# Kernel tuning notes

Measured on AMD Instinct MI355X. Metric: run time of the kernel, lower is better.

The kernel has to match this reference:

```python
import jax, jax.numpy as jnp
import numpy as np

H = 64  # LSTM units for both layers
T = 128  # sequence length
D = 128  # input feature dim
B = 2048  # batch

def setup_inputs() -> dict:
    key = jax.random.key(0)
    ks = jax.random.split(key, 7)
    s_in = 1.0 / np.sqrt(D)
    s_h = 1.0 / np.sqrt(H)
    return {
        "x": jax.random.normal(ks[0], (B, T, D), dtype=jnp.float32),
        # Keras LSTM weights: kernel [in, 4H], recurrent_kernel [H, 4H], bias [4H]
        # gate order: i, f, g (cell candidate), o
        "W1": jax.random.normal(ks[1], (D, 4 * H), dtype=jnp.float32) * s_in,
        "U1": jax.random.normal(ks[2], (H, 4 * H), dtype=jnp.float32) * s_h,
        "b1": jnp.zeros((4 * H,), dtype=jnp.float32),
        "W2": jax.random.normal(ks[3], (H, 4 * H), dtype=jnp.float32) * s_h,
        "U2": jax.random.normal(ks[4], (H, 4 * H), dtype=jnp.float32) * s_h,
        "b2": jnp.zeros((4 * H,), dtype=jnp.float32),
    }

def _lstm(x, W, U, b, act):
    """Keras-faithful LSTM, return_sequences=True, zero init state.
    x: [B, T, D_in] -> hs: [B, T, H]
    recurrent_activation = sigmoid; `act` is the cell/output activation.
    """
    Bsz = x.shape[0]
    # Precompute input projections for all timesteps (one big GEMM).
    xz = jnp.einsum('btd,dg->btg', x, W) + b  # [B, T, 4H]
    xz = jnp.swapaxes(xz, 0, 1)  # [T, B, 4H]

    def step(carry, zt):
        h, c = carry
        z = zt + h @ U  # [B, 4H]
        i, f, g, o = jnp.split(z, 4, axis=-1)
        i = jax.nn.sigmoid(i)
        f = jax.nn.sigmoid(f)
        g = act(g)
        o = jax.nn.sigmoid(o)
        c = f * c + i * g
        h = o * act(c)
        return (h, c), h

    init = (jnp.zeros((Bsz, H), x.dtype), jnp.zeros((Bsz, H), x.dtype))
    _, hs = jax.lax.scan(step, init, xz)  # hs: [T, B, H]
    return jnp.swapaxes(hs, 0, 1)  # [B, T, H]

def reference(x, W1, U1, b1, W2, U2, b2):
    h1 = _lstm(x, W1, U1, b1, jnp.tanh)           # layer 1: default tanh
    h2 = _lstm(h1, W2, U2, b2, jax.nn.sigmoid)    # layer 2: activation='sigmoid'
    return h2.reshape(h2.shape[0], T * H, 1)      # Reshape((8192, 1))
```

## Files before the change

### kernel.cpp

```cpp
#include <hip/hip_runtime.h>
#include <stdint.h>

typedef __attribute__((ext_vector_type(8))) short short8;
typedef __attribute__((ext_vector_type(4))) short short4_t;
typedef __attribute__((ext_vector_type(4))) float floatx4;

#define TT 128
#define DD 128

#define BARRIER_LDS() asm volatile("s_waitcnt lgkmcnt(0)\n\ts_barrier" ::: "memory")

__device__ __forceinline__ short f2bf(float f) {
  union { float f; uint32_t u; } v; v.f = f;
  uint32_t u = v.u;
  u += 0x7fffu + ((u >> 16) & 1u);
  return (short)(u >> 16);
}

__device__ __forceinline__ float sigf(float x) {
  return __builtin_amdgcn_rcpf(1.f + __expf(-x));
}
__device__ __forceinline__ float tanhf_(float x) {
  return 2.f * __builtin_amdgcn_rcpf(1.f + __expf(-2.f * x)) - 1.f;
}

__global__ void wtrans_all(const float* __restrict__ W1, const float* __restrict__ U1,
                           const float* __restrict__ W2, const float* __restrict__ U2,
                           short* __restrict__ w1t, short* __restrict__ u1t,
                           short* __restrict__ w2t, short* __restrict__ u2t) {
  int n = blockIdx.x;
  int k = threadIdx.x;
  w1t[n * 128 + k] = f2bf(W1[k * 256 + n]);
  if (k < 64) {
    u1t[n * 64 + k] = f2bf(U1[k * 256 + n]);
    w2t[n * 64 + k] = f2bf(W2[k * 256 + n]);
    u2t[n * 64 + k] = f2bf(U2[k * 256 + n]);
  }
}

__global__ __launch_bounds__(512, 2) void lstm_fused(
    const float* __restrict__ x,
    const short* __restrict__ w1t, const short* __restrict__ u1t,
    const short* __restrict__ w2t, const short* __restrict__ u2t,
    const float* __restrict__ b1, const float* __restrict__ b2,
    float* __restrict__ out) {
  __shared__ short hb1[2][8 * 80];
  __shared__ short hb2[2][8 * 80];
  __shared__ short xbuf[2][8 * 144];

  const int tid = threadIdx.x;
  const int w = tid >> 6;
  const bool isL1 = (w < 4);
  const int wg = w & 3;
  const int lane = tid & 63;
  const int mrow = lane & 15;
  const int quad = lane >> 4;
  const int rowbase = blockIdx.x * 8;
  const int colw = wg * 16 + mrow;
  const int br_a = 2 * (mrow >> 2) + (mrow & 1);

  short8 wA[4][4], uA[4][2];
  float bias[4];
  if (isL1) {
#pragma unroll
    for (int g = 0; g < 4; ++g) {
      const int n = g * 4 + wg;
#pragma unroll
      for (int s = 0; s < 4; ++s)
        wA[g][s] = *(const short8*)(w1t + n * 2048 + mrow * 128 + quad * 8 + s * 32);
#pragma unroll
      for (int s = 0; s < 2; ++s)
        uA[g][s] = *(const short8*)(u1t + n * 1024 + mrow * 64 + quad * 8 + s * 32);
      bias[g] = b1[g * 64 + colw];
    }
  } else {
#pragma unroll
    for (int g = 0; g < 4; ++g) {
      const int n = g * 4 + wg;
#pragma unroll
      for (int s = 0; s < 2; ++s) {
        wA[g][s]     = *(const short8*)(w2t + n * 1024 + mrow * 64 + quad * 8 + s * 32);
        wA[g][2 + s] = *(const short8*)(u2t + n * 1024 + mrow * 64 + quad * 8 + s * 32);
      }
      bias[g] = b2[g * 64 + colw];
    }
  }

  const int tid2 = tid & 255;
  const int sxr = tid2 >> 5;
  const int sxc = (tid2 & 31) * 4;
  const float* xload = x + (size_t)(rowbase + sxr) * (TT * DD) + sxc;

  short8 h1f[2], xh[4];
  float cc[2] = {0.f, 0.f};
  floatx4 xcur, xnxt;

  for (int idx = tid; idx < 2 * 8 * 80; idx += 512) {
    ((short*)hb1)[idx] = 0;
    ((short*)hb2)[idx] = 0;
  }
  if (!isL1) {
    floatx4 x0 = *(const floatx4*)xload;
    short4_t v;
#pragma unroll
    for (int j = 0; j < 4; ++j) v[j] = f2bf(x0[j]);
    *(short4_t*)&xbuf[0][sxr * 144 + sxc] = v;
    xcur = *(const floatx4*)(xload + DD);
    xnxt = *(const floatx4*)(xload + 2 * DD);
  }
  BARRIER_LDS();

  float* outp = out + (size_t)rowbase * 8192 + colw;

#pragma unroll 1
  for (int i = 0; i <= TT; ++i) {
    const int p = i & 1;

    if (isL1) {
      if (i < TT) {
#pragma unroll
        for (int s = 0; s < 4; ++s)
          xh[s] = *(const short8*)&xbuf[p][br_a * 144 + (quad + 4 * s) * 8];
        h1f[0] = *(const short8*)&hb1[1 - p][br_a * 80 + quad * 8];
        h1f[1] = *(const short8*)&hb1[1 - p][br_a * 80 + (quad + 4) * 8];

        floatx4 acc[4];
#pragma unroll
        for (int g = 0; g < 4; ++g) acc[g] = floatx4{0.f, 0.f, 0.f, 0.f};
#pragma unroll
        for (int s = 0; s < 4; ++s)
#pragma unroll
          for (int g = 0; g < 4; ++g)
            acc[g] = __builtin_amdgcn_mfma_f32_16x16x32_bf16(xh[s], wA[g][s], acc[g], 0, 0, 0);
#pragma unroll
        for (int s = 0; s < 2; ++s)
#pragma unroll
          for (int g = 0; g < 4; ++g)
            acc[g] = __builtin_amdgcn_mfma_f32_16x16x32_bf16(h1f[s], uA[g][s], acc[g], 0, 0, 0);

#pragma unroll
        for (int r = 0; r < 2; ++r) {
          float ig = sigf(acc[0][r] + bias[0]);
          float fg = sigf(acc[1][r] + bias[1]);
          float gg = tanhf_(acc[2][r] + bias[2]);
          float og = sigf(acc[3][r] + bias[3]);
          float c = fg * cc[r] + ig * gg;
          cc[r] = c;
          float h = og * tanhf_(c);
          hb1[p][(2 * quad + r) * 80 + colw] = f2bf(h);
        }
      }
    } else {
      if (i >= 1) {
        h1f[0] = *(const short8*)&hb1[1 - p][br_a * 80 + quad * 8];
        h1f[1] = *(const short8*)&hb1[1 - p][br_a * 80 + (quad + 4) * 8];
        xh[0]  = *(const short8*)&hb2[1 - p][br_a * 80 + quad * 8];
        xh[1]  = *(const short8*)&hb2[1 - p][br_a * 80 + (quad + 4) * 8];

        floatx4 acc[4];
#pragma unroll
        for (int g = 0; g < 4; ++g) acc[g] = floatx4{0.f, 0.f, 0.f, 0.f};
#pragma unroll
        for (int s = 0; s < 2; ++s)
#pragma unroll
          for (int g = 0; g < 4; ++g)
            acc[g] = __builtin_amdgcn_mfma_f32_16x16x32_bf16(h1f[s], wA[g][s], acc[g], 0, 0, 0);
#pragma unroll
        for (int s = 0; s < 2; ++s)
#pragma unroll
          for (int g = 0; g < 4; ++g)
            acc[g] = __builtin_amdgcn_mfma_f32_16x16x32_bf16(xh[s], wA[g][2 + s], acc[g], 0, 0, 0);

        if (i <= TT - 2) {
          short4_t v;
#pragma unroll
          for (int j = 0; j < 4; ++j) v[j] = f2bf(xcur[j]);
          *(short4_t*)&xbuf[1 - p][sxr * 144 + sxc] = v;
          xcur = xnxt;
          const int tn = (i + 3 < TT) ? (i + 3) : (TT - 1);
          xnxt = *(const floatx4*)(xload + (size_t)tn * DD);
        }

        const int t = i - 1;
#pragma unroll
        for (int r = 0; r < 2; ++r) {
          float ig = sigf(acc[0][r] + bias[0]);
          float fg = sigf(acc[1][r] + bias[1]);
          float gg = sigf(acc[2][r] + bias[2]);
          float og = sigf(acc[3][r] + bias[3]);
          float c = fg * cc[r] + ig * gg;
          cc[r] = c;
          float h = og * sigf(c);
          hb2[p][(2 * quad + r) * 80 + colw] = f2bf(h);
          outp[(size_t)(2 * quad + r) * 8192 + t * 64] = h;
        }
      } else {
        short4_t v;
#pragma unroll
        for (int j = 0; j < 4; ++j) v[j] = f2bf(xcur[j]);
        *(short4_t*)&xbuf[1 - p][sxr * 144 + sxc] = v;
        xcur = xnxt;
        xnxt = *(const floatx4*)(xload + (size_t)3 * DD);
      }
    }

    BARRIER_LDS();
  }
}

extern "C" void kernel_launch(void* const* d_in, const int* in_sizes, int n_in,
                              void* d_out, int out_size, void* d_ws, size_t ws_size,
                              hipStream_t stream) {
  const float* x  = (const float*)d_in[0];
  const float* W1 = (const float*)d_in[1];
  const float* U1 = (const float*)d_in[2];
  const float* b1 = (const float*)d_in[3];
  const float* W2 = (const float*)d_in[4];
  const float* U2 = (const float*)d_in[5];
  const float* b2 = (const float*)d_in[6];
  float* out = (float*)d_out;

  short* w1t = (short*)d_ws;
  short* u1t = w1t + 32768;
  short* w2t = u1t + 16384;
  short* u2t = w2t + 16384;

  hipLaunchKernelGGL(wtrans_all, dim3(256), dim3(128), 0, stream,
                     W1, U1, W2, U2, w1t, u1t, w2t, u2t);
  hipLaunchKernelGGL(lstm_fused, dim3(256), dim3(512), 0, stream,
                     x, w1t, u1t, w2t, u2t, b1, b2, out);
}
```

Baseline: 327.7 us.

## Software-pipeline layer-1 input projection one step ahead of the recurrence

Layer-1 waves now compute the x·W input-projection MFMAs for step t+1 after finishing the gate update for step t, so each step's critical path holds only the recurrent h·U MFMAs. To support this, the layer-2 waves stage x into LDS one step further ahead, with a two-deep register prefetch and a prologue that preloads two timesteps. Scheduling fences are added before the barriers to keep the compiler from moving work across them. The accumulators now live across loop iterations, which raises register pressure under the 512-thread, 2-block launch bounds.

```diff
diff --git a/kernel.cpp b/kernel.cpp
--- a/kernel.cpp
+++ b/kernel.cpp
@@ -9,6 +9,7 @@
 #define DD 128
 
 #define BARRIER_LDS() asm volatile("s_waitcnt lgkmcnt(0)\n\ts_barrier" ::: "memory")
+#define SFENCE() __builtin_amdgcn_sched_barrier(0)
 
 __device__ __forceinline__ short f2bf(float f) {
   union { float f; uint32_t u; } v; v.f = f;
@@ -92,8 +93,9 @@
   const float* xload = x + (size_t)(rowbase + sxr) * (TT * DD) + sxc;
 
   short8 h1f[2], xh[4];
+  floatx4 acc[4];
   float cc[2] = {0.f, 0.f};
-  floatx4 xcur, xnxt;
+  floatx4 xn_a, xn_b;
 
   for (int idx = tid; idx < 2 * 8 * 80; idx += 512) {
     ((short*)hb1)[idx] = 0;
@@ -101,13 +103,31 @@
   }
   if (!isL1) {
     floatx4 x0 = *(const floatx4*)xload;
+    floatx4 x1 = *(const floatx4*)(xload + DD);
     short4_t v;
 #pragma unroll
     for (int j = 0; j < 4; ++j) v[j] = f2bf(x0[j]);
     *(short4_t*)&xbuf[0][sxr * 144 + sxc] = v;
-    xcur = *(const floatx4*)(xload + DD);
-    xnxt = *(const floatx4*)(xload + 2 * DD);
-  }
+#pragma unroll
+    for (int j = 0; j < 4; ++j) v[j] = f2bf(x1[j]);
+    *(short4_t*)&xbuf[1][sxr * 144 + sxc] = v;
+    xn_a = *(const floatx4*)(xload + 2 * DD);
+    xn_b = *(const floatx4*)(xload + 3 * DD);
+  }
+  BARRIER_LDS();
+  if (isL1) {
+#pragma unroll
+    for (int s = 0; s < 4; ++s)
+      xh[s] = *(const short8*)&xbuf[0][br_a * 144 + (quad + 4 * s) * 8];
+#pragma unroll
+    for (int g = 0; g < 4; ++g) acc[g] = floatx4{0.f, 0.f, 0.f, 0.f};
+#pragma unroll
+    for (int s = 0; s < 4; ++s)
+#pragma unroll
+      for (int g = 0; g < 4; ++g)
+        acc[g] = __builtin_amdgcn_mfma_f32_16x16x32_bf16(xh[s], wA[g][s], acc[g], 0, 0, 0);
+  }
+  SFENCE();
   BARRIER_LDS();
 
   float* outp = out + (size_t)rowbase * 8192 + colw;
@@ -118,26 +138,13 @@
 
     if (isL1) {
       if (i < TT) {
-#pragma unroll
-        for (int s = 0; s < 4; ++s)
-          xh[s] = *(const short8*)&xbuf[p][br_a * 144 + (quad + 4 * s) * 8];
         h1f[0] = *(const short8*)&hb1[1 - p][br_a * 80 + quad * 8];
         h1f[1] = *(const short8*)&hb1[1 - p][br_a * 80 + (quad + 4) * 8];
-
-        floatx4 acc[4];
-#pragma unroll
-        for (int g = 0; g < 4; ++g) acc[g] = floatx4{0.f, 0.f, 0.f, 0.f};
-#pragma unroll
-        for (int s = 0; s < 4; ++s)
-#pragma unroll
-          for (int g = 0; g < 4; ++g)
-            acc[g] = __builtin_amdgcn_mfma_f32_16x16x32_bf16(xh[s], wA[g][s], acc[g], 0, 0, 0);
 #pragma unroll
         for (int s = 0; s < 2; ++s)
 #pragma unroll
           for (int g = 0; g < 4; ++g)
             acc[g] = __builtin_amdgcn_mfma_f32_16x16x32_bf16(h1f[s], uA[g][s], acc[g], 0, 0, 0);
-
 #pragma unroll
         for (int r = 0; r < 2; ++r) {
           float ig = sigf(acc[0][r] + bias[0]);
@@ -150,14 +157,24 @@
           hb1[p][(2 * quad + r) * 80 + colw] = f2bf(h);
         }
       }
+      if (i <= TT - 2) {
+#pragma unroll
+        for (int s = 0; s < 4; ++s)
+          xh[s] = *(const short8*)&xbuf[1 - p][br_a * 144 + (quad + 4 * s) * 8];
+#pragma unroll
+        for (int g = 0; g < 4; ++g) acc[g] = floatx4{0.f, 0.f, 0.f, 0.f};
+#pragma unroll
+        for (int s = 0; s < 4; ++s)
+#pragma unroll
+          for (int g = 0; g < 4; ++g)
+            acc[g] = __builtin_amdgcn_mfma_f32_16x16x32_bf16(xh[s], wA[g][s], acc[g], 0, 0, 0);
+      }
     } else {
       if (i >= 1) {
         h1f[0] = *(const short8*)&hb1[1 - p][br_a * 80 + quad * 8];
         h1f[1] = *(const short8*)&hb1[1 - p][br_a * 80 + (quad + 4) * 8];
-        xh[0]  = *(const short8*)&hb2[1 - p][br_a * 80 + quad * 8];
-        xh[1]  = *(const short8*)&hb2[1 - p][br_a * 80 + (quad + 4) * 8];
-
-        floatx4 acc[4];
+        short8 g2a = *(const short8*)&hb2[1 - p][br_a * 80 + quad * 8];
+        short8 g2b = *(const short8*)&hb2[1 - p][br_a * 80 + (quad + 4) * 8];
 #pragma unroll
         for (int g = 0; g < 4; ++g) acc[g] = floatx4{0.f, 0.f, 0.f, 0.f};
 #pragma unroll
@@ -166,21 +183,11 @@
           for (int g = 0; g < 4; ++g)
             acc[g] = __builtin_amdgcn_mfma_f32_16x16x32_bf16(h1f[s], wA[g][s], acc[g], 0, 0, 0);
 #pragma unroll
-        for (int s = 0; s < 2; ++s)
-#pragma unroll
-          for (int g = 0; g < 4; ++g)
-            acc[g] = __builtin_amdgcn_mfma_f32_16x16x32_bf16(xh[s], wA[g][2 + s], acc[g], 0, 0, 0);
-
-        if (i <= TT - 2) {
-          short4_t v;
-#pragma unroll
-          for (int j = 0; j < 4; ++j) v[j] = f2bf(xcur[j]);
-          *(short4_t*)&xbuf[1 - p][sxr * 144 + sxc] = v;
-          xcur = xnxt;
-          const int tn = (i + 3 < TT) ? (i + 3) : (TT - 1);
-          xnxt = *(const floatx4*)(xload + (size_t)tn * DD);
-        }
-
+        for (int g = 0; g < 4; ++g)
+          acc[g] = __builtin_amdgcn_mfma_f32_16x16x32_bf16(g2a, wA[g][2], acc[g], 0, 0, 0);
+#pragma unroll
+        for (int g = 0; g < 4; ++g)
+          acc[g] = __builtin_amdgcn_mfma_f32_16x16x32_bf16(g2b, wA[g][3], acc[g], 0, 0, 0);
         const int t = i - 1;
 #pragma unroll
         for (int r = 0; r < 2; ++r) {
@@ -194,16 +201,19 @@
           hb2[p][(2 * quad + r) * 80 + colw] = f2bf(h);
           outp[(size_t)(2 * quad + r) * 8192 + t * 64] = h;
         }
-      } else {
+      }
+      if (i <= TT - 3) {
         short4_t v;
 #pragma unroll
-        for (int j = 0; j < 4; ++j) v[j] = f2bf(xcur[j]);
-        *(short4_t*)&xbuf[1 - p][sxr * 144 + sxc] = v;
-        xcur = xnxt;
-        xnxt = *(const floatx4*)(xload + (size_t)3 * DD);
+        for (int j = 0; j < 4; ++j) v[j] = f2bf(xn_a[j]);
+        *(short4_t*)&xbuf[p][sxr * 144 + sxc] = v;
+        xn_a = xn_b;
+        const int tn = (i + 4 < TT) ? (i + 4) : (TT - 1);
+        xn_b = *(const floatx4*)(xload + (size_t)tn * DD);
       }
     }
 
+    SFENCE();
     BARRIER_LDS();
   }
 }
```

Result: slower. 344.2 us (+5.1%).
